# Optimization experiments

Measured on AMD Instinct MI355X. Metric: run time of the kernel, lower is better.

Reference implementation:

```python
import jax, jax.numpy as jnp
import numpy as np

N = 50000   # nodes
E = 300000  # edges per etype
D = 256     # in_channels
STEPS = 3   # number_steps
EPS = 1e-5  # LayerNorm eps


def setup_inputs() -> dict:
    key = jax.random.key(0)
    ks = jax.random.split(key, 32)
    inp = {"x": jax.random.normal(ks[0], (N, D), jnp.float32)}
    for e in range(4):
        inp[f"src{e}"] = jax.random.randint(ks[1 + 2 * e], (E,), 0, N)
        inp[f"dst{e}"] = jax.random.randint(ks[2 + 2 * e], (E,), 0, N)
        inp[f"W{e}"] = jax.random.normal(ks[9 + e], (D, D), jnp.float32) / np.sqrt(D).astype(np.float32)
        inp[f"b{e}"] = jnp.zeros((D,), jnp.float32)
    inp["W_ih"] = jax.random.normal(ks[20], (3 * D, D), jnp.float32) / np.sqrt(D).astype(np.float32)
    inp["W_hh"] = jax.random.normal(ks[21], (3 * D, D), jnp.float32) / np.sqrt(D).astype(np.float32)
    inp["b_ih"] = jnp.zeros((3 * D,), jnp.float32)
    inp["b_hh"] = jnp.zeros((3 * D,), jnp.float32)
    inp["gamma"] = jnp.ones((D,), jnp.float32)
    inp["beta"] = jnp.zeros((D,), jnp.float32)
    return inp


def reference(x, src0, dst0, src1, dst1, src2, dst2, src3, dst3,
              W0, b0, W1, b1, W2, b2, W3, b3,
              W_ih, W_hh, b_ih, b_hh, gamma, beta):
    srcs = (src0, src1, src2, src3)
    dsts = (dst0, dst1, dst2, dst3)
    lins = ((W0, b0), (W1, b1), (W2, b2), (W3, b3))
    n_nodes = x.shape[0]

    def step(h):
        # per-etype: linear projection, gather on src, scatter-mean on dst; cross-etype 'sum'
        agg = jnp.zeros_like(h)
        for (W, b), s, d in zip(lins, srcs, dsts):
            proj = h @ W.T + b                                  # [N, D]
            msum = jax.ops.segment_sum(proj[s], d, num_segments=n_nodes)  # [N, D]
            deg = jax.ops.segment_sum(jnp.ones((s.shape[0], 1), h.dtype), d, num_segments=n_nodes)
            agg = agg + msum / jnp.maximum(deg, 1.0)            # mean; 0 for isolated nodes
        # torch GRUCell: input = agg, hidden = h
        gi = agg @ W_ih.T + b_ih                                # [N, 3D]
        gh = h @ W_hh.T + b_hh                                  # [N, 3D]
        i_r, i_z, i_n = jnp.split(gi, 3, axis=-1)
        h_r, h_z, h_n = jnp.split(gh, 3, axis=-1)
        r = jax.nn.sigmoid(i_r + h_r)
        z = jax.nn.sigmoid(i_z + h_z)
        n = jnp.tanh(i_n + r * h_n)
        h = (1.0 - z) * n + z * h
        # LayerNorm (use_norm=True); dropout is identity in eval mode
        mu = h.mean(-1, keepdims=True)
        var = h.var(-1, keepdims=True)
        return (h - mu) * jax.lax.rsqrt(var + EPS) * gamma + beta

    for _ in range(STEPS):
        x = step(x)
    return x
```

## Files before the change

### kernel.cpp

```cpp
#include <hip/hip_runtime.h>
#include <hip/hip_bf16.h>
#include <cstddef>

#define N_NODES 50000
#define E_EDGES 300000
#define D 256
#define M_PAD 50048
#define SCHUNKS 196

typedef unsigned short u16;
typedef __attribute__((ext_vector_type(8))) short bf16x8;
typedef __attribute__((ext_vector_type(4))) float f32x4;

__device__ __forceinline__ float b2f(u16 u) {
    return __uint_as_float(((unsigned)u) << 16);
}
__device__ __forceinline__ u16 f2b(float f) {
    __hip_bfloat16 h = __float2bfloat16(f);
    return *reinterpret_cast<u16*>(&h);
}
__device__ __forceinline__ void async16(const u16* g, u16* l) {
    __builtin_amdgcn_global_load_lds(
        (const __attribute__((address_space(1))) void*)g,
        (__attribute__((address_space(3))) void*)l, 16, 0, 0);
}

__global__ __launch_bounds__(256) void prep_kernel(
    const float* __restrict__ W0, const float* __restrict__ W1,
    const float* __restrict__ W2, const float* __restrict__ W3,
    const float* __restrict__ b0, const float* __restrict__ b1,
    const float* __restrict__ b2, const float* __restrict__ b3,
    const float* __restrict__ W_ih, const float* __restrict__ W_hh,
    const float* __restrict__ b_ih, const float* __restrict__ b_hh,
    u16* __restrict__ Bfull_b, u16* __restrict__ Bcat_b,
    u16* __restrict__ WnH_b,
    float* __restrict__ bfull, float* __restrict__ be4)
{
    int t = blockIdx.x * 256 + threadIdx.x;
    if (t < 393216) {
        int j = t >> 9, k = t & 511;
        float v;
        if (k < 256)      v = W_ih[j * 256 + k];
        else if (j < 512) v = W_hh[j * 256 + (k - 256)];
        else              v = 0.f;
        Bfull_b[t] = f2b(v);
    }
    if (t < 262144) {
        int p = t >> 17, rem = t & 131071;
        int j = rem >> 9, k = rem & 511;
        int e = p * 2 + (k >> 8), kk = k & 255;
        const float* W = (e == 0) ? W0 : (e == 1) ? W1 : (e == 2) ? W2 : W3;
        Bcat_b[t] = f2b(W[j * 256 + kk]);
    }
    if (t < 65536) WnH_b[t] = f2b(W_hh[131072 + t]);
    if (t < 768)   bfull[t] = b_ih[t] + (t < 512 ? b_hh[t] : 0.f);
    if (t < 1024) {
        int e = t >> 8, k = t & 255;
        const float* b = (e == 0) ? b0 : (e == 1) ? b1 : (e == 2) ? b2 : b3;
        be4[t] = b[k];
    }
}

__global__ __launch_bounds__(256) void xcvt_kernel(
    const float* __restrict__ x, u16* __restrict__ hb)
{
    int t = blockIdx.x * 256 + threadIdx.x;
    float4 v = *reinterpret_cast<const float4*>(x + (size_t)t * 4);
    ushort4 o;
    o.x = f2b(v.x); o.y = f2b(v.y); o.z = f2b(v.z); o.w = f2b(v.w);
    *reinterpret_cast<ushort4*>(hb + (size_t)t * 4) = o;
}

__global__ __launch_bounds__(256) void cnt_kernel(
    const int* __restrict__ d0, const int* __restrict__ d1,
    const int* __restrict__ d2, const int* __restrict__ d3,
    int* __restrict__ rowptr)
{
    int i = blockIdx.x * 256 + threadIdx.x;
    if (i >= 4 * E_EDGES) return;
    int e = i / E_EDGES;
    int k = i - e * E_EDGES;
    const int* dp = (e == 0) ? d0 : (e == 1) ? d1 : (e == 2) ? d2 : d3;
    atomicAdd(&rowptr[e * (N_NODES + 1) + dp[k] + 1], 1);
}

__global__ __launch_bounds__(256) void scan1_kernel(
    int* __restrict__ rowptr, int* __restrict__ bsum)
{
    int e = blockIdx.y;
    int blk = blockIdx.x;
    int t = threadIdx.x;
    int idx = blk * 256 + t;
    int* rp = rowptr + e * (N_NODES + 1);
    int v = (idx <= N_NODES) ? rp[idx] : 0;
    __shared__ int s[256];
    s[t] = v;
    __syncthreads();
    for (int o = 1; o < 256; o <<= 1) {
        int u = (t >= o) ? s[t - o] : 0;
        __syncthreads();
        s[t] += u;
        __syncthreads();
    }
    if (idx <= N_NODES) rp[idx] = s[t];
    if (t == 255) bsum[e * SCHUNKS + blk] = s[255];
}

__global__ __launch_bounds__(256) void scan2_kernel(int* __restrict__ bsum)
{
    int e = blockIdx.x;
    int t = threadIdx.x;
    int v = (t < SCHUNKS) ? bsum[e * SCHUNKS + t] : 0;
    __shared__ int s[256];
    s[t] = v;
    __syncthreads();
    for (int o = 1; o < 256; o <<= 1) {
        int u = (t >= o) ? s[t - o] : 0;
        __syncthreads();
        s[t] += u;
        __syncthreads();
    }
    if (t < SCHUNKS) bsum[e * SCHUNKS + t] = s[t];
}

__global__ __launch_bounds__(256) void scan3_kernel(
    int* __restrict__ rowptr, const int* __restrict__ bsum)
{
    int e = blockIdx.y;
    int blk = blockIdx.x;
    if (blk == 0) return;
    int idx = blk * 256 + threadIdx.x;
    if (idx > N_NODES) return;
    rowptr[e * (N_NODES + 1) + idx] += bsum[e * SCHUNKS + blk - 1];
}

__global__ __launch_bounds__(256) void fill_csr_kernel(
    const int* __restrict__ s0, const int* __restrict__ d0,
    const int* __restrict__ s1, const int* __restrict__ d1,
    const int* __restrict__ s2, const int* __restrict__ d2,
    const int* __restrict__ s3, const int* __restrict__ d3,
    int* __restrict__ rowptr, u16* __restrict__ colb)
{
    int i = blockIdx.x * 256 + threadIdx.x;
    if (i >= 4 * E_EDGES) return;
    int e = i / E_EDGES;
    int k = i - e * E_EDGES;
    const int* sp = (e == 0) ? s0 : (e == 1) ? s1 : (e == 2) ? s2 : s3;
    const int* dp = (e == 0) ? d0 : (e == 1) ? d1 : (e == 2) ? d2 : d3;
    int dst = dp[k];
    int slot = atomicAdd(&rowptr[e * (N_NODES + 1) + dst], 1);
    colb[(size_t)e * E_EDGES + slot] = (u16)sp[k];
}

__global__ __launch_bounds__(256) void degmask_kernel(
    const int* __restrict__ rowptr, unsigned char* __restrict__ degmask)
{
    int n = blockIdx.x * 256 + threadIdx.x;
    if (n >= N_NODES) return;
    int m = 0;
#pragma unroll
    for (int e = 0; e < 4; ++e) {
        const int* rp = rowptr + e * (N_NODES + 1);
        int beg = n ? rp[n - 1] : 0;
        if (rp[n] > beg) m |= (1 << e);
    }
    degmask[n] = (unsigned char)m;
}

__global__ __launch_bounds__(256) void gather2_kernel(
    const u16* __restrict__ hb, const int* __restrict__ rowptr,
    const u16* __restrict__ colb, u16* __restrict__ Hmean2, int pair)
{
    int n = blockIdx.x * 2 + (threadIdx.x >> 7);
    int el = (threadIdx.x >> 6) & 1;
    int lane = threadIdx.x & 63;
    int e = pair * 2 + el;
    const int* rp = rowptr + e * (N_NODES + 1);
    int beg = n ? rp[n - 1] : 0;
    int end = rp[n];
    const u16* cb = colb + (size_t)e * E_EDGES;

    float4 a0 = make_float4(0.f, 0.f, 0.f, 0.f);
    float4 a1 = a0, a2 = a0, a3 = a0;
    int j = beg;
    for (; j + 4 <= end; j += 4) {
        int s0 = cb[j], s1 = cb[j + 1], s2 = cb[j + 2], s3 = cb[j + 3];
        ushort4 u0 = *reinterpret_cast<const ushort4*>(hb + (size_t)s0 * D + lane * 4);
        ushort4 u1 = *reinterpret_cast<const ushort4*>(hb + (size_t)s1 * D + lane * 4);
        ushort4 u2 = *reinterpret_cast<const ushort4*>(hb + (size_t)s2 * D + lane * 4);
        ushort4 u3 = *reinterpret_cast<const ushort4*>(hb + (size_t)s3 * D + lane * 4);
        a0.x += b2f(u0.x); a0.y += b2f(u0.y); a0.z += b2f(u0.z); a0.w += b2f(u0.w);
        a1.x += b2f(u1.x); a1.y += b2f(u1.y); a1.z += b2f(u1.z); a1.w += b2f(u1.w);
        a2.x += b2f(u2.x); a2.y += b2f(u2.y); a2.z += b2f(u2.z); a2.w += b2f(u2.w);
        a3.x += b2f(u3.x); a3.y += b2f(u3.y); a3.z += b2f(u3.z); a3.w += b2f(u3.w);
    }
    for (; j < end; ++j) {
        int s0 = cb[j];
        ushort4 u0 = *reinterpret_cast<const ushort4*>(hb + (size_t)s0 * D + lane * 4);
        a0.x += b2f(u0.x); a0.y += b2f(u0.y); a0.z += b2f(u0.z); a0.w += b2f(u0.w);
    }
    float ax = (a0.x + a1.x) + (a2.x + a3.x);
    float ay = (a0.y + a1.y) + (a2.y + a3.y);
    float az = (a0.z + a1.z) + (a2.z + a3.z);
    float aw = (a0.w + a1.w) + (a2.w + a3.w);
    float s = (end > beg) ? 1.f / (float)(end - beg) : 0.f;
    ushort4 o;
    o.x = f2b(ax * s); o.y = f2b(ay * s); o.z = f2b(az * s); o.w = f2b(aw * s);
    *reinterpret_cast<ushort4*>(Hmean2 + (size_t)n * 512 + el * 256 + lane * 4) = o;
}

template <int BIASK, bool ACCUM>
__global__ __launch_bounds__(256) void gemm_mfma(
    const u16* __restrict__ A0, int lda0,
    const u16* __restrict__ A1, int lda1,
    const u16* __restrict__ Bw,
    u16* __restrict__ C0, int ldc0, u16* __restrict__ C1, int ldc1, int split,
    int K, int KS,
    const float* __restrict__ bias0, const float* __restrict__ bias1,
    const unsigned char* __restrict__ degmask, int mshift)
{
    __shared__ u16 As[8192];
    __shared__ u16 Bs2[8192];

    const int gx = gridDim.x;
    const int nwg = gx * gridDim.y;
    const int lin = blockIdx.y * gx + blockIdx.x;
    const int q = nwg >> 3, r = nwg & 7;
    const int xcd = lin & 7, pos = lin >> 3;
    const int wg = (xcd < r) ? xcd * (q + 1) + pos
                             : r * (q + 1) + (xcd - r) * q + pos;
    const int by = wg / gx;
    const int bx = wg - by * gx;
    const int bm = by * 128;
    const int bn = bx * 128;

    const int tid = threadIdx.x;
    const int lane = tid & 63;
    const int wid = tid >> 6;
    const int wr = wid >> 1;
    const int wc = wid & 1;
    const int l15 = lane & 15;
    const int l4 = lane >> 4;

    int srow[4], schk[4];
#pragma unroll
    for (int i = 0; i < 4; ++i) {
        int qq = (wid * 4 + i) * 64 + lane;
        srow[i] = qq >> 3;
        schk[i] = (qq & 7) ^ (srow[i] & 7);
    }

    f32x4 acc[4][4];
#pragma unroll
    for (int i = 0; i < 4; ++i)
#pragma unroll
        for (int j = 0; j < 4; ++j)
            acc[i][j] = (f32x4){0.f, 0.f, 0.f, 0.f};

    const int nkt = (bn < split) ? (K >> 6) : KS;
    for (int kt = 0; kt < nkt; ++kt) {
        const u16* Ab = (kt < KS) ? A0 + (size_t)kt * 64
                                  : A1 + (size_t)(kt - KS) * 64;
        const int lda = (kt < KS) ? lda0 : lda1;
#pragma unroll
        for (int i = 0; i < 4; ++i)
            async16(Ab + (size_t)(bm + srow[i]) * lda + schk[i] * 8,
                    &As[(wid * 4 + i) * 512]);
#pragma unroll
        for (int i = 0; i < 4; ++i)
            async16(Bw + (size_t)(bn + srow[i]) * K + kt * 64 + schk[i] * 8,
                    &Bs2[(wid * 4 + i) * 512]);
        __syncthreads();

#pragma unroll
        for (int kk = 0; kk < 2; ++kk) {
            bf16x8 a[4], b[4];
#pragma unroll
            for (int i = 0; i < 4; ++i) {
                int ar = wr * 64 + i * 16 + l15;
                a[i] = *reinterpret_cast<const bf16x8*>(
                    &As[ar * 64 + (((kk * 4 + l4) ^ (ar & 7)) << 3)]);
                int bc = wc * 64 + i * 16 + l15;
                b[i] = *reinterpret_cast<const bf16x8*>(
                    &Bs2[bc * 64 + (((kk * 4 + l4) ^ (bc & 7)) << 3)]);
            }
#pragma unroll
            for (int i = 0; i < 4; ++i)
#pragma unroll
                for (int j = 0; j < 4; ++j)
                    acc[i][j] = __builtin_amdgcn_mfma_f32_16x16x32_bf16(
                        a[i], b[j], acc[i][j], 0, 0, 0);
        }
        __syncthreads();
    }

    u16* Cw; int ldc, cb0;
    if (bn < split) { Cw = C0; ldc = ldc0; cb0 = bn; }
    else            { Cw = C1; ldc = ldc1; cb0 = bn - split; }

    float bj0[4], bj1[4];
#pragma unroll
    for (int j = 0; j < 4; ++j) {
        int col = bn + wc * 64 + j * 16 + l15;
        bj0[j] = bias0[col];
        if (BIASK == 3) bj1[j] = bias1[col];
    }
#pragma unroll
    for (int i = 0; i < 4; ++i) {
        int row0 = bm + wr * 64 + i * 16 + l4 * 4;
#pragma unroll
        for (int r2 = 0; r2 < 4; ++r2) {
            int row = row0 + r2;
            if (row < N_NODES) {
                float m0 = 1.f, m1 = 0.f;
                if (BIASK == 3) {
                    int bits = degmask[row] >> mshift;
                    m0 = (bits & 1) ? 1.f : 0.f;
                    m1 = (bits & 2) ? 1.f : 0.f;
                }
#pragma unroll
                for (int j = 0; j < 4; ++j) {
                    int col = cb0 + wc * 64 + j * 16 + l15;
                    float o = acc[i][j][r2];
                    if (BIASK == 3) o += m0 * bj0[j] + m1 * bj1[j];
                    else            o += bj0[j];
                    u16* cp = Cw + (size_t)row * ldc + col;
                    if (ACCUM) o += b2f(*cp);
                    *cp = f2b(o);
                }
            }
        }
    }
}

template <int OUTM>
__global__ __launch_bounds__(256) void gru_ln_kernel(
    const u16* __restrict__ rz, const u16* __restrict__ nin,
    const u16* __restrict__ hn, const u16* __restrict__ hb,
    void* __restrict__ outv,
    const float* __restrict__ gamma, const float* __restrict__ beta)
{
    int w = threadIdx.x >> 6;
    int l = threadIdx.x & 63;
    int n = blockIdx.x * 4 + w;
    size_t b2 = (size_t)n * 512;
    size_t b1 = (size_t)n * D;

    u16 ra[4], za[4], na[4], ha[4], va[4];
    *reinterpret_cast<ushort4*>(ra) = *reinterpret_cast<const ushort4*>(rz + b2 + l * 4);
    *reinterpret_cast<ushort4*>(za) = *reinterpret_cast<const ushort4*>(rz + b2 + 256 + l * 4);
    *reinterpret_cast<ushort4*>(na) = *reinterpret_cast<const ushort4*>(nin + b1 + l * 4);
    *reinterpret_cast<ushort4*>(ha) = *reinterpret_cast<const ushort4*>(hn + b1 + l * 4);
    *reinterpret_cast<ushort4*>(va) = *reinterpret_cast<const ushort4*>(hb + b1 + l * 4);

    float hnew[4];
    float s1 = 0.f, s2 = 0.f;
#pragma unroll
    for (int c = 0; c < 4; ++c) {
        float r = 1.f / (1.f + __expf(-b2f(ra[c])));
        float z = 1.f / (1.f + __expf(-b2f(za[c])));
        float xn = b2f(na[c]) + r * b2f(ha[c]);
        float nn = 2.f / (1.f + __expf(-2.f * xn)) - 1.f;
        hnew[c] = (1.f - z) * nn + z * b2f(va[c]);
        s1 += hnew[c];
        s2 += hnew[c] * hnew[c];
    }
#pragma unroll
    for (int o = 32; o > 0; o >>= 1) {
        s1 += __shfl_down(s1, o);
        s2 += __shfl_down(s2, o);
    }
    float sum = __shfl(s1, 0);
    float ssq = __shfl(s2, 0);
    float mu = sum * (1.f / D);
    float var = ssq * (1.f / D) - mu * mu;
    float rstd = rsqrtf(var + 1e-5f);

    float4 g = *reinterpret_cast<const float4*>(gamma + l * 4);
    float4 bt = *reinterpret_cast<const float4*>(beta + l * 4);
    float res[4];
    res[0] = (hnew[0] - mu) * rstd * g.x + bt.x;
    res[1] = (hnew[1] - mu) * rstd * g.y + bt.y;
    res[2] = (hnew[2] - mu) * rstd * g.z + bt.z;
    res[3] = (hnew[3] - mu) * rstd * g.w + bt.w;

    if (OUTM == 0) {
        ushort4 o;
        o.x = f2b(res[0]); o.y = f2b(res[1]); o.z = f2b(res[2]); o.w = f2b(res[3]);
        *reinterpret_cast<ushort4*>((u16*)outv + b1 + l * 4) = o;
    } else {
        *reinterpret_cast<float4*>((float*)outv + b1 + l * 4) =
            make_float4(res[0], res[1], res[2], res[3]);
    }
}

__global__ __launch_bounds__(256) void wsfail_kernel(float* __restrict__ out, float val, int n)
{
    int i = blockIdx.x * 256 + threadIdx.x;
    if (i < n) out[i] = val;
}

extern "C" void kernel_launch(void* const* d_in, const int* in_sizes, int n_in,
                              void* d_out, int out_size, void* d_ws, size_t ws_size,
                              hipStream_t stream)
{
    const float* x    = (const float*)d_in[0];
    const int* se[4] = {(const int*)d_in[1], (const int*)d_in[5],
                        (const int*)d_in[9], (const int*)d_in[13]};
    const int* de[4] = {(const int*)d_in[2], (const int*)d_in[6],
                        (const int*)d_in[10], (const int*)d_in[14]};
    const float* We[4] = {(const float*)d_in[3], (const float*)d_in[7],
                          (const float*)d_in[11], (const float*)d_in[15]};
    const float* be[4] = {(const float*)d_in[4], (const float*)d_in[8],
                          (const float*)d_in[12], (const float*)d_in[16]};
    const float* W_ih = (const float*)d_in[17];
    const float* W_hh = (const float*)d_in[18];
    const float* b_ih = (const float*)d_in[19];
    const float* b_hh = (const float*)d_in[20];
    const float* gamma = (const float*)d_in[21];
    const float* beta  = (const float*)d_in[22];
    float* outf = (float*)d_out;

    char* base = (char*)d_ws;
    size_t off = 0;
    u16* Hmean2 = (u16*)(base + off); off += (size_t)M_PAD * 512 * 2;
    u16* rzb    = Hmean2;
    u16* aggb = (u16*)(base + off); off += (size_t)M_PAD * 256 * 2;
    u16* hnb  = aggb;
    u16* ninb = (u16*)(base + off); off += (size_t)N_NODES * 256 * 2;
    u16* h_bf = (u16*)(base + off); off += (size_t)M_PAD * 256 * 2;
    int* rowptr = (int*)(base + off); off += (size_t)4 * (N_NODES + 1) * 4;
    u16* colb = (u16*)(base + off); off += (size_t)4 * E_EDGES * 2;
    unsigned char* degmask = (unsigned char*)(base + off); off += 50048;
    int* bsum = (int*)(base + off); off += (size_t)4 * SCHUNKS * 4;
    u16* Bfull_b = (u16*)(base + off); off += 786432;
    u16* Bcat_b  = (u16*)(base + off); off += 524288;
    u16* WnH_b   = (u16*)(base + off); off += 131072;
    float* bfull = (float*)(base + off); off += 3072;
    float* be4   = (float*)(base + off); off += 4096;

    if (ws_size < off) {
        wsfail_kernel<<<(out_size + 255) / 256, 256, 0, stream>>>(
            outf, (float)(ws_size >> 20), out_size);
        return;
    }

    hipMemsetAsync(rowptr, 0, (size_t)4 * (N_NODES + 1) * 4, stream);
    hipMemsetAsync(Hmean2 + (size_t)N_NODES * 512, 0, (size_t)(M_PAD - N_NODES) * 512 * 2, stream);
    hipMemsetAsync(aggb + (size_t)N_NODES * 256, 0, (size_t)(M_PAD - N_NODES) * 256 * 2, stream);
    hipMemsetAsync(h_bf + (size_t)N_NODES * 256, 0, (size_t)(M_PAD - N_NODES) * 256 * 2, stream);
    prep_kernel<<<1536, 256, 0, stream>>>(
        We[0], We[1], We[2], We[3], be[0], be[1], be[2], be[3],
        W_ih, W_hh, b_ih, b_hh, Bfull_b, Bcat_b, WnH_b, bfull, be4);
    xcvt_kernel<<<N_NODES * D / 4 / 256, 256, 0, stream>>>(x, h_bf);
    cnt_kernel<<<(4 * E_EDGES + 255) / 256, 256, 0, stream>>>(
        de[0], de[1], de[2], de[3], rowptr);
    scan1_kernel<<<dim3(SCHUNKS, 4), 256, 0, stream>>>(rowptr, bsum);
    scan2_kernel<<<4, 256, 0, stream>>>(bsum);
    scan3_kernel<<<dim3(SCHUNKS, 4), 256, 0, stream>>>(rowptr, bsum);
    fill_csr_kernel<<<(4 * E_EDGES + 255) / 256, 256, 0, stream>>>(
        se[0], de[0], se[1], de[1], se[2], de[2], se[3], de[3], rowptr, colb);
    degmask_kernel<<<(N_NODES + 255) / 256, 256, 0, stream>>>(rowptr, degmask);

    const dim3 g2(2, 391), g6(6, 391);
    for (int step = 0; step < 3; ++step) {
        gather2_kernel<<<N_NODES / 2, 256, 0, stream>>>(h_bf, rowptr, colb, Hmean2, 0);
        gemm_mfma<3, false><<<g2, 256, 0, stream>>>(
            Hmean2, 512, nullptr, 0, Bcat_b, aggb, 256, aggb, 256, 256,
            512, 8, be4, be4 + 256, degmask, 0);
        gather2_kernel<<<N_NODES / 2, 256, 0, stream>>>(h_bf, rowptr, colb, Hmean2, 1);
        gemm_mfma<3, true><<<g2, 256, 0, stream>>>(
            Hmean2, 512, nullptr, 0, Bcat_b + 131072, aggb, 256, aggb, 256, 256,
            512, 8, be4 + 512, be4 + 768, degmask, 2);

        gemm_mfma<1, false><<<g6, 256, 0, stream>>>(
            aggb, 256, h_bf, 256, Bfull_b, rzb, 512, ninb, 256, 512,
            512, 4, bfull, nullptr, nullptr, 0);
        gemm_mfma<1, false><<<g2, 256, 0, stream>>>(
            h_bf, 256, nullptr, 0, WnH_b, hnb, 256, hnb, 256, 256,
            256, 4, b_hh + 512, nullptr, nullptr, 0);

        if (step < 2)
            gru_ln_kernel<0><<<N_NODES / 4, 256, 0, stream>>>(
                rzb, ninb, hnb, h_bf, h_bf, gamma, beta);
        else
            gru_ln_kernel<1><<<N_NODES / 4, 256, 0, stream>>>(
                rzb, ninb, hnb, h_bf, outf, gamma, beta);
    }
}
```

Before: 946.4 us.

## Fuse per-pair gathers and GEMMs into single K=1024 launch, merge GRU GEMMs

When the workspace is large enough, all four edge types are gathered in one launch into a 1024-wide buffer, and a single K=1024 GEMM produces the aggregate with per-etype masked biases. The two GRU GEMMs are merged into one 8-column-block launch that writes three outputs. This cuts kernel launches and avoids re-reading and accumulating the agg buffer. CSR fill now uses ranks recorded during counting instead of a second atomic pass. Row padding and its memsets are replaced by clamping rows in the loads, and a fallback path is kept for small workspaces.

After: 813.1 us. 1.16x faster.

```diff
diff --git a/kernel.cpp b/kernel.cpp
--- a/kernel.cpp
+++ b/kernel.cpp
@@ -5,7 +5,6 @@
 #define N_NODES 50000
 #define E_EDGES 300000
 #define D 256
-#define M_PAD 50048
 #define SCHUNKS 196
 
 typedef unsigned short u16;
@@ -33,28 +32,25 @@
     const float* __restrict__ W_ih, const float* __restrict__ W_hh,
     const float* __restrict__ b_ih, const float* __restrict__ b_hh,
     u16* __restrict__ Bfull_b, u16* __restrict__ Bcat_b,
-    u16* __restrict__ WnH_b,
     float* __restrict__ bfull, float* __restrict__ be4)
 {
     int t = blockIdx.x * 256 + threadIdx.x;
-    if (t < 393216) {
+    {
         int j = t >> 9, k = t & 511;
         float v;
-        if (k < 256)      v = W_ih[j * 256 + k];
-        else if (j < 512) v = W_hh[j * 256 + (k - 256)];
-        else              v = 0.f;
+        if (k < 256) v = (j < 768) ? W_ih[j * 256 + k] : W_hh[(j - 256) * 256 + k];
+        else         v = (j < 512) ? W_hh[j * 256 + (k - 256)] : 0.f;
         Bfull_b[t] = f2b(v);
     }
     if (t < 262144) {
-        int p = t >> 17, rem = t & 131071;
-        int j = rem >> 9, k = rem & 511;
-        int e = p * 2 + (k >> 8), kk = k & 255;
+        int j = t >> 10, k = t & 1023;
+        int e = k >> 8, kk = k & 255;
         const float* W = (e == 0) ? W0 : (e == 1) ? W1 : (e == 2) ? W2 : W3;
         Bcat_b[t] = f2b(W[j * 256 + kk]);
     }
-    if (t < 65536) WnH_b[t] = f2b(W_hh[131072 + t]);
-    if (t < 768)   bfull[t] = b_ih[t] + (t < 512 ? b_hh[t] : 0.f);
     if (t < 1024) {
+        bfull[t] = (t < 512) ? b_ih[t] + b_hh[t]
+                 : (t < 768) ? b_ih[t] : b_hh[t - 256];
         int e = t >> 8, k = t & 255;
         const float* b = (e == 0) ? b0 : (e == 1) ? b1 : (e == 2) ? b2 : b3;
         be4[t] = b[k];
@@ -74,14 +70,14 @@
 __global__ __launch_bounds__(256) void cnt_kernel(
     const int* __restrict__ d0, const int* __restrict__ d1,
     const int* __restrict__ d2, const int* __restrict__ d3,
-    int* __restrict__ rowptr)
+    int* __restrict__ rowptr, u16* __restrict__ rank)
 {
     int i = blockIdx.x * 256 + threadIdx.x;
     if (i >= 4 * E_EDGES) return;
     int e = i / E_EDGES;
     int k = i - e * E_EDGES;
     const int* dp = (e == 0) ? d0 : (e == 1) ? d1 : (e == 2) ? d2 : d3;
-    atomicAdd(&rowptr[e * (N_NODES + 1) + dp[k] + 1], 1);
+    rank[i] = (u16)atomicAdd(&rowptr[e * (N_NODES + 1) + dp[k] + 1], 1);
 }
 
 __global__ __launch_bounds__(256) void scan1_kernel(
@@ -139,7 +135,8 @@
     const int* __restrict__ s1, const int* __restrict__ d1,
     const int* __restrict__ s2, const int* __restrict__ d2,
     const int* __restrict__ s3, const int* __restrict__ d3,
-    int* __restrict__ rowptr, u16* __restrict__ colb)
+    const int* __restrict__ rowptr, const u16* __restrict__ rank,
+    u16* __restrict__ colb)
 {
     int i = blockIdx.x * 256 + threadIdx.x;
     if (i >= 4 * E_EDGES) return;
@@ -148,7 +145,7 @@
     const int* sp = (e == 0) ? s0 : (e == 1) ? s1 : (e == 2) ? s2 : s3;
     const int* dp = (e == 0) ? d0 : (e == 1) ? d1 : (e == 2) ? d2 : d3;
     int dst = dp[k];
-    int slot = atomicAdd(&rowptr[e * (N_NODES + 1) + dst], 1);
+    int slot = rowptr[e * (N_NODES + 1) + dst] + (int)rank[i];
     colb[(size_t)e * E_EDGES + slot] = (u16)sp[k];
 }
 
@@ -161,23 +158,23 @@
 #pragma unroll
     for (int e = 0; e < 4; ++e) {
         const int* rp = rowptr + e * (N_NODES + 1);
-        int beg = n ? rp[n - 1] : 0;
-        if (rp[n] > beg) m |= (1 << e);
+        if (rp[n + 1] > rp[n]) m |= (1 << e);
     }
     degmask[n] = (unsigned char)m;
 }
 
-__global__ __launch_bounds__(256) void gather2_kernel(
+__global__ __launch_bounds__(256) void gather_kernel(
     const u16* __restrict__ hb, const int* __restrict__ rowptr,
-    const u16* __restrict__ colb, u16* __restrict__ Hmean2, int pair)
-{
+    const u16* __restrict__ colb, u16* __restrict__ out,
+    int pairArg, int stride)
+{
+    int p = (pairArg < 0) ? (int)blockIdx.y : pairArg;
     int n = blockIdx.x * 2 + (threadIdx.x >> 7);
     int el = (threadIdx.x >> 6) & 1;
     int lane = threadIdx.x & 63;
-    int e = pair * 2 + el;
+    int e = p * 2 + el;
     const int* rp = rowptr + e * (N_NODES + 1);
-    int beg = n ? rp[n - 1] : 0;
-    int end = rp[n];
+    int beg = rp[n], end = rp[n + 1];
     const u16* cb = colb + (size_t)e * E_EDGES;
 
     float4 a0 = make_float4(0.f, 0.f, 0.f, 0.f);
@@ -204,18 +201,20 @@
     float az = (a0.z + a1.z) + (a2.z + a3.z);
     float aw = (a0.w + a1.w) + (a2.w + a3.w);
     float s = (end > beg) ? 1.f / (float)(end - beg) : 0.f;
+    int colblk = (stride == 1024) ? e : el;
     ushort4 o;
     o.x = f2b(ax * s); o.y = f2b(ay * s); o.z = f2b(az * s); o.w = f2b(aw * s);
-    *reinterpret_cast<ushort4*>(Hmean2 + (size_t)n * 512 + el * 256 + lane * 4) = o;
+    *reinterpret_cast<ushort4*>(out + (size_t)n * stride + colblk * 256 + lane * 4) = o;
 }
 
 template <int BIASK, bool ACCUM>
 __global__ __launch_bounds__(256) void gemm_mfma(
     const u16* __restrict__ A0, int lda0,
     const u16* __restrict__ A1, int lda1,
-    const u16* __restrict__ Bw,
-    u16* __restrict__ C0, int ldc0, u16* __restrict__ C1, int ldc1, int split,
-    int K, int KS,
+    const u16* __restrict__ Bw, int ldb,
+    u16* __restrict__ C0, int ldc0, u16* __restrict__ C1, int ldc1,
+    u16* __restrict__ C2, int ldc2,
+    int split1, int split2, int nkt0, int KS,
     const float* __restrict__ bias0, const float* __restrict__ bias1,
     const unsigned char* __restrict__ degmask, int mshift)
 {
@@ -257,18 +256,25 @@
         for (int j = 0; j < 4; ++j)
             acc[i][j] = (f32x4){0.f, 0.f, 0.f, 0.f};
 
-    const int nkt = (bn < split) ? (K >> 6) : KS;
+    int nkt, ksel;
+    if (bn < split1)      { nkt = nkt0; ksel = KS; }
+    else if (bn < split2) { nkt = KS;   ksel = KS; }
+    else                  { nkt = KS;   ksel = 0;  }
+
     for (int kt = 0; kt < nkt; ++kt) {
-        const u16* Ab = (kt < KS) ? A0 + (size_t)kt * 64
-                                  : A1 + (size_t)(kt - KS) * 64;
-        const int lda = (kt < KS) ? lda0 : lda1;
+        const u16* Ab; int lda;
+        if (kt < ksel) { Ab = A0 + (size_t)kt * 64;          lda = lda0; }
+        else           { Ab = A1 + (size_t)(kt - ksel) * 64; lda = lda1; }
+#pragma unroll
+        for (int i = 0; i < 4; ++i) {
+            int rrow = bm + srow[i];
+            if (rrow > N_NODES - 1) rrow = N_NODES - 1;
+            async16(Ab + (size_t)rrow * lda + schk[i] * 8,
+                    &As[(wid * 4 + i) * 512]);
+        }
 #pragma unroll
         for (int i = 0; i < 4; ++i)
-            async16(Ab + (size_t)(bm + srow[i]) * lda + schk[i] * 8,
-                    &As[(wid * 4 + i) * 512]);
-#pragma unroll
-        for (int i = 0; i < 4; ++i)
-            async16(Bw + (size_t)(bn + srow[i]) * K + kt * 64 + schk[i] * 8,
+            async16(Bw + (size_t)(bn + srow[i]) * ldb + kt * 64 + schk[i] * 8,
                     &Bs2[(wid * 4 + i) * 512]);
         __syncthreads();
 
@@ -295,15 +301,25 @@
     }
 
     u16* Cw; int ldc, cb0;
-    if (bn < split) { Cw = C0; ldc = ldc0; cb0 = bn; }
-    else            { Cw = C1; ldc = ldc1; cb0 = bn - split; }
+    if (bn < split1)      { Cw = C0; ldc = ldc0; cb0 = bn; }
+    else if (bn < split2) { Cw = C1; ldc = ldc1; cb0 = bn - split1; }
+    else                  { Cw = C2; ldc = ldc2; cb0 = bn - split2; }
 
     float bj0[4], bj1[4];
-#pragma unroll
-    for (int j = 0; j < 4; ++j) {
-        int col = bn + wc * 64 + j * 16 + l15;
-        bj0[j] = bias0[col];
-        if (BIASK == 3) bj1[j] = bias1[col];
+    float bj4[4][4];
+    if constexpr (BIASK == 4) {
+#pragma unroll
+        for (int e = 0; e < 4; ++e)
+#pragma unroll
+            for (int j = 0; j < 4; ++j)
+                bj4[e][j] = bias0[e * 256 + bn + wc * 64 + j * 16 + l15];
+    } else {
+#pragma unroll
+        for (int j = 0; j < 4; ++j) {
+            int col = bn + wc * 64 + j * 16 + l15;
+            bj0[j] = bias0[col];
+            if (BIASK == 3) bj1[j] = bias1[col];
+        }
     }
 #pragma unroll
     for (int i = 0; i < 4; ++i) {
@@ -312,18 +328,21 @@
         for (int r2 = 0; r2 < 4; ++r2) {
             int row = row0 + r2;
             if (row < N_NODES) {
-                float m0 = 1.f, m1 = 0.f;
-                if (BIASK == 3) {
-                    int bits = degmask[row] >> mshift;
-                    m0 = (bits & 1) ? 1.f : 0.f;
-                    m1 = (bits & 2) ? 1.f : 0.f;
-                }
 #pragma unroll
                 for (int j = 0; j < 4; ++j) {
                     int col = cb0 + wc * 64 + j * 16 + l15;
                     float o = acc[i][j][r2];
-                    if (BIASK == 3) o += m0 * bj0[j] + m1 * bj1[j];
-                    else            o += bj0[j];
+                    if constexpr (BIASK == 4) {
+                        int bits = degmask[row];
+#pragma unroll
+                        for (int e = 0; e < 4; ++e)
+                            o += ((bits >> e) & 1) ? bj4[e][j] : 0.f;
+                    } else if constexpr (BIASK == 3) {
+                        int bits = degmask[row] >> mshift;
+                        o += ((bits & 1) ? bj0[j] : 0.f) + ((bits & 2) ? bj1[j] : 0.f);
+                    } else {
+                        o += bj0[j];
+                    }
                     u16* cp = Cw + (size_t)row * ldc + col;
                     if (ACCUM) o += b2f(*cp);
                     *cp = f2b(o);
@@ -421,64 +440,101 @@
     const float* beta  = (const float*)d_in[22];
     float* outf = (float*)d_out;
 
-    char* base = (char*)d_ws;
-    size_t off = 0;
-    u16* Hmean2 = (u16*)(base + off); off += (size_t)M_PAD * 512 * 2;
-    u16* rzb    = Hmean2;
-    u16* aggb = (u16*)(base + off); off += (size_t)M_PAD * 256 * 2;
-    u16* hnb  = aggb;
-    u16* ninb = (u16*)(base + off); off += (size_t)N_NODES * 256 * 2;
-    u16* h_bf = (u16*)(base + off); off += (size_t)M_PAD * 256 * 2;
-    int* rowptr = (int*)(base + off); off += (size_t)4 * (N_NODES + 1) * 4;
-    u16* colb = (u16*)(base + off); off += (size_t)4 * E_EDGES * 2;
-    unsigned char* degmask = (unsigned char*)(base + off); off += 50048;
-    int* bsum = (int*)(base + off); off += (size_t)4 * SCHUNKS * 4;
-    u16* Bfull_b = (u16*)(base + off); off += 786432;
-    u16* Bcat_b  = (u16*)(base + off); off += 524288;
-    u16* WnH_b   = (u16*)(base + off); off += 131072;
-    float* bfull = (float*)(base + off); off += 3072;
-    float* be4   = (float*)(base + off); off += 4096;
-
-    if (ws_size < off) {
+    const size_t SZ_H4 = (size_t)N_NODES * 1024 * 2;
+    const size_t SZ_H2 = (size_t)N_NODES * 512 * 2;
+    const size_t SZ_ND = (size_t)N_NODES * 256 * 2;
+    const size_t TAIL = 800016 + 3136 + 2400000 + 2400000 + 50000
+                      + 1048576 + 524288 + 4096 + 4096;
+    const size_t NEED_BIG   = SZ_H4 + 2 * SZ_ND + TAIL;
+    const size_t NEED_SMALL = SZ_H2 + 3 * SZ_ND + TAIL;
+
+    const bool big = (ws_size >= NEED_BIG);
+
+    char* p = (char*)d_ws;
+    u16 *Hm, *rzb, *ninb, *hnb, *aggb, *h_bf;
+    if (big) {
+        Hm   = (u16*)p; p += SZ_H4;
+        rzb  = Hm;
+        ninb = (u16*)((char*)Hm + SZ_H2);
+        hnb  = (u16*)((char*)Hm + SZ_H2 + SZ_ND);
+        aggb = (u16*)p; p += SZ_ND;
+        h_bf = (u16*)p; p += SZ_ND;
+    } else {
+        Hm   = (u16*)p; p += SZ_H2;
+        rzb  = Hm;
+        aggb = (u16*)p; p += SZ_ND;
+        hnb  = aggb;
+        ninb = (u16*)p; p += SZ_ND;
+        h_bf = (u16*)p; p += SZ_ND;
+    }
+    int* rowptr = (int*)p; p += 800016;
+    int* bsum   = (int*)p; p += 3136;
+    u16* colb   = (u16*)p; p += 2400000;
+    u16* rank   = (u16*)p; p += 2400000;
+    unsigned char* degmask = (unsigned char*)p; p += 50000;
+    u16* Bfull_b = (u16*)p; p += 1048576;
+    u16* Bcat_b  = (u16*)p; p += 524288;
+    float* bfull = (float*)p; p += 4096;
+    float* be4   = (float*)p; p += 4096;
+
+    if (ws_size < (size_t)(p - (char*)d_ws)) {
         wsfail_kernel<<<(out_size + 255) / 256, 256, 0, stream>>>(
             outf, (float)(ws_size >> 20), out_size);
         return;
     }
 
     hipMemsetAsync(rowptr, 0, (size_t)4 * (N_NODES + 1) * 4, stream);
-    hipMemsetAsync(Hmean2 + (size_t)N_NODES * 512, 0, (size_t)(M_PAD - N_NODES) * 512 * 2, stream);
-    hipMemsetAsync(aggb + (size_t)N_NODES * 256, 0, (size_t)(M_PAD - N_NODES) * 256 * 2, stream);
-    hipMemsetAsync(h_bf + (size_t)N_NODES * 256, 0, (size_t)(M_PAD - N_NODES) * 256 * 2, stream);
-    prep_kernel<<<1536, 256, 0, stream>>>(
+    prep_kernel<<<2048, 256, 0, stream>>>(
         We[0], We[1], We[2], We[3], be[0], be[1], be[2], be[3],
-        W_ih, W_hh, b_ih, b_hh, Bfull_b, Bcat_b, WnH_b, bfull, be4);
+        W_ih, W_hh, b_ih, b_hh, Bfull_b, Bcat_b, bfull, be4);
     xcvt_kernel<<<N_NODES * D / 4 / 256, 256, 0, stream>>>(x, h_bf);
     cnt_kernel<<<(4 * E_EDGES + 255) / 256, 256, 0, stream>>>(
-        de[0], de[1], de[2], de[3], rowptr);
+        de[0], de[1], de[2], de[3], rowptr, rank);
     scan1_kernel<<<dim3(SCHUNKS, 4), 256, 0, stream>>>(rowptr, bsum);
     scan2_kernel<<<4, 256, 0, stream>>>(bsum);
     scan3_kernel<<<dim3(SCHUNKS, 4), 256, 0, stream>>>(rowptr, bsum);
     fill_csr_kernel<<<(4 * E_EDGES + 255) / 256, 256, 0, stream>>>(
-        se[0], de[0], se[1], de[1], se[2], de[2], se[3], de[3], rowptr, colb);
+        se[0], de[0], se[1], de[1], se[2], de[2], se[3], de[3],
+        rowptr, rank, colb);
     degmask_kernel<<<(N_NODES + 255) / 256, 256, 0, stream>>>(rowptr, degmask);
 
-    const dim3 g2(2, 391), g6(6, 391);
+    const int BIG30 = 1 << 30;
     for (int step = 0; step < 3; ++step) {
-        gather2_kernel<<<N_NODES / 2, 256, 0, stream>>>(h_bf, rowptr, colb, Hmean2, 0);
-        gemm_mfma<3, false><<<g2, 256, 0, stream>>>(
-            Hmean2, 512, nullptr, 0, Bcat_b, aggb, 256, aggb, 256, 256,
-            512, 8, be4, be4 + 256, degmask, 0);
-        gather2_kernel<<<N_NODES / 2, 256, 0, stream>>>(h_bf, rowptr, colb, Hmean2, 1);
-        gemm_mfma<3, true><<<g2, 256, 0, stream>>>(
-            Hmean2, 512, nullptr, 0, Bcat_b + 131072, aggb, 256, aggb, 256, 256,
-            512, 8, be4 + 512, be4 + 768, degmask, 2);
-
-        gemm_mfma<1, false><<<g6, 256, 0, stream>>>(
-            aggb, 256, h_bf, 256, Bfull_b, rzb, 512, ninb, 256, 512,
-            512, 4, bfull, nullptr, nullptr, 0);
-        gemm_mfma<1, false><<<g2, 256, 0, stream>>>(
-            h_bf, 256, nullptr, 0, WnH_b, hnb, 256, hnb, 256, 256,
-            256, 4, b_hh + 512, nullptr, nullptr, 0);
+        if (big) {
+            gather_kernel<<<dim3(N_NODES / 2, 2), 256, 0, stream>>>(
+                h_bf, rowptr, colb, Hm, -1, 1024);
+            gemm_mfma<4, false><<<dim3(2, 391), 256, 0, stream>>>(
+                Hm, 1024, nullptr, 0, Bcat_b, 1024,
+                aggb, 256, nullptr, 0, nullptr, 0,
+                BIG30, BIG30, 16, 16, be4, nullptr, degmask, 0);
+            gemm_mfma<1, false><<<dim3(8, 391), 256, 0, stream>>>(
+                aggb, 256, h_bf, 256, Bfull_b, 512,
+                rzb, 512, ninb, 256, hnb, 256,
+                512, 768, 8, 4, bfull, nullptr, nullptr, 0);
+        } else {
+            for (int pair = 0; pair < 2; ++pair) {
+                gather_kernel<<<dim3(N_NODES / 2, 1), 256, 0, stream>>>(
+                    h_bf, rowptr, colb, Hm, pair, 512);
+                if (pair == 0)
+                    gemm_mfma<3, false><<<dim3(2, 391), 256, 0, stream>>>(
+                        Hm, 512, nullptr, 0, Bcat_b + 512, 1024,
+                        aggb, 256, nullptr, 0, nullptr, 0,
+                        BIG30, BIG30, 8, 8, be4, be4 + 256, degmask, 0);
+                else
+                    gemm_mfma<3, true><<<dim3(2, 391), 256, 0, stream>>>(
+                        Hm, 512, nullptr, 0, Bcat_b + 512, 1024,
+                        aggb, 256, nullptr, 0, nullptr, 0,
+                        BIG30, BIG30, 8, 8, be4 + 512, be4 + 768, degmask, 2);
+            }
+            gemm_mfma<1, false><<<dim3(6, 391), 256, 0, stream>>>(
+                aggb, 256, h_bf, 256, Bfull_b, 512,
+                rzb, 512, ninb, 256, nullptr, 0,
+                512, BIG30, 8, 4, bfull, nullptr, nullptr, 0);
+            gemm_mfma<1, false><<<dim3(2, 391), 256, 0, stream>>>(
+                nullptr, 0, h_bf, 256, Bfull_b + (size_t)768 * 512, 512,
+                nullptr, 0, nullptr, 0, hnb, 256,
+                0, 0, 4, 4, bfull + 768, nullptr, nullptr, 0);
+        }
 
         if (step < 2)
             gru_ln_kernel<0><<<N_NODES / 4, 256, 0, stream>>>(
```
